# Optimization experiments

Measured on AMD Instinct MI355X. Metric: run time of the kernel, lower is better.

Reference implementation:

```python
import jax, jax.numpy as jnp
import numpy as np

EPS = 1e-6


def setup_inputs() -> dict:
    key = jax.random.key(0)
    kx, kw = jax.random.split(key)
    B, C, N = 8, 256, 2048
    x = jax.random.normal(kx, (B, C, N), dtype=jnp.float32)
    # nn.Linear(dim*2, 2, bias=False): weight shape [2, 2*C]
    W = jax.random.normal(kw, (2, 2 * C), dtype=jnp.float32) * (1.0 / np.sqrt(2 * C))
    return {"x": x, "W": W}


def reference(x, W):
    B, C, N = x.shape
    # cosine similarity matrix [B, N, N]
    sim = jnp.einsum('bcn,bcm->bnm', x, x)
    # torch: sqrt(sum(x^2 + 1e-6, dim=1)) -> eps added per-channel before sum
    norms = jnp.sqrt(jnp.sum(x * x + EPS, axis=1))            # [B, N]
    io_abs = sim / (norms[:, :, None] * norms[:, None, :])    # [B, N, N]
    # zero the diagonal (fill_diagonal_(0)) before argmax
    io_abs = io_abs * (1.0 - jnp.eye(N, dtype=io_abs.dtype))
    idx = jnp.argmax(io_abs, axis=2)                          # [B, N] nearest-neighbor per token
    # gather retrieved features: f_re[b, :, n] = x[b, :, idx[b, n]]
    f_re = jnp.take_along_axis(x, idx[:, None, :], axis=2)    # [B, C, N]
    # gated fusion
    fus = jnp.concatenate([x, f_re], axis=1).transpose(0, 2, 1)  # [B, N, 2C]
    w = jax.nn.softmax(fus @ W.T, axis=-1)                    # [B, N, 2]
    w = w.transpose(0, 2, 1)                                  # [B, 2, N]
    out = x * w[:, 0:1, :] + f_re * w[:, 1:2, :]
    return (out, f_re)
```

## Files before the change

kernel.cpp:

```cpp
#include <hip/hip_runtime.h>
#include <hip/hip_bf16.h>
#include <math.h>

constexpr int B_ = 8;
constexpr int C_ = 256;
constexpr int N_ = 2048;
constexpr int CN_ = C_ * N_;
constexpr int TOT_ = B_ * C_ * N_;
constexpr int NTILES = 16;
constexpr int NPAIRS = 136;

typedef __attribute__((ext_vector_type(8))) short bf16x8;
typedef __attribute__((ext_vector_type(4))) float f32x4;

__device__ __forceinline__ void g2l16(const void* g, void* l) {
    __builtin_amdgcn_global_load_lds(
        (const __attribute__((address_space(1))) void*)g,
        (__attribute__((address_space(3))) void*)l, 16, 0, 0);
}

__device__ __forceinline__ unsigned short bits(__hip_bfloat16 h) {
    union { __hip_bfloat16 b; unsigned short u; } cv;
    cv.b = h;
    return cv.u;
}

__device__ __forceinline__ float b2f(short s) {
    union { float f; unsigned u; } cv;
    cv.u = ((unsigned)(unsigned short)s) << 16;
    return cv.f;
}

__global__ __launch_bounds__(256) void convert_kernel(const float* __restrict__ x,
                                                      __hip_bfloat16* __restrict__ hiT,
                                                      __hip_bfloat16* __restrict__ loT,
                                                      float* __restrict__ normacc) {
    const int blk = blockIdx.x;
    const int batch = blk & 7;
    const int nt = (blk >> 3) & 31;
    const int ctile = blk >> 8;
    const int n0 = nt << 6, c0 = ctile << 6;
    const int t = threadIdx.x;
    const int i = t & 63, j = t >> 6;

    __shared__ float tb[64][65];
    __shared__ float red[4][64];

    float s = 0.f;
    const float* xp = x + (size_t)batch * CN_ + (size_t)c0 * N_ + n0 + i;
#pragma unroll 4
    for (int r = 0; r < 16; ++r) {
        const int cl = j + r * 4;
        const float v = xp[(size_t)cl * N_];
        tb[cl][i] = v;
        s += v * v;
    }
    red[j][i] = s;
    __syncthreads();

    const int cp = t & 31;
    const int c2 = cp << 1;
    const int nb = t >> 5;
#pragma unroll 4
    for (int r = 0; r < 8; ++r) {
        const int n = nb + r * 8;
        const float v0 = tb[c2][n], v1 = tb[c2 + 1][n];
        const size_t o = ((size_t)batch * N_ + n0 + n) * C_ + c0 + c2;
        const __hip_bfloat16 h0 = __float2bfloat16(v0);
        const __hip_bfloat16 h1 = __float2bfloat16(v1);
        const __hip_bfloat16 g0 = __float2bfloat16(v0 - __bfloat162float(h0));
        const __hip_bfloat16 g1 = __float2bfloat16(v1 - __bfloat162float(h1));
        ((unsigned*)hiT)[o >> 1] = ((unsigned)bits(h1) << 16) | bits(h0);
        ((unsigned*)loT)[o >> 1] = ((unsigned)bits(g1) << 16) | bits(g0);
    }
    if (j == 0) {
        const float tt = red[0][i] + red[1][i] + red[2][i] + red[3][i];
        atomicAdd(normacc + batch * N_ + n0 + i, tt);
    }
}

__global__ void rnorm_fin_kernel(const float* __restrict__ normacc,
                                 float* __restrict__ rnorm) {
    const int t = blockIdx.x * 256 + threadIdx.x;
    rnorm[t] = 1.0f / sqrtf(normacc[t] + 256.0f * 1e-6f);
}

__device__ __forceinline__ void stage_tile(const __hip_bfloat16* __restrict__ hiT,
                                           const __hip_bfloat16* __restrict__ loT,
                                           size_t base, int kb, short* dst, int tid) {
#pragma unroll
    for (int pp = 0; pp < 4; ++pp) {
        const int slot = tid + pp * 256;
        const int r = slot >> 3, sidx = slot & 7;
        const int sw = sidx ^ (r & 7);
        const size_t goff = base + (size_t)r * C_ + kb + (sw & 3) * 8;
        const __hip_bfloat16* src = (sw < 4) ? (hiT + goff) : (loT + goff);
        g2l16(src, dst + slot * 8);
    }
}

__global__ __launch_bounds__(256, 2) void gram_mfma_kernel(
        const __hip_bfloat16* __restrict__ hiT, const __hip_bfloat16* __restrict__ loT,
        const float* __restrict__ rnorm,
        float* __restrict__ pval, int* __restrict__ pidx, float* __restrict__ pval2) {
    const int blk = blockIdx.x;
    const int batch = blk & 7;
    int p = blk >> 3;
    int bn = 0;
    while (p >= NTILES - bn) { p -= NTILES - bn; ++bn; }
    const int bm = bn + p;
    const bool diag = (bn == bm);
    const int n0 = bn << 7, m0 = bm << 7;

    __shared__ short As[2][128 * 64];
    __shared__ short Bs[2][128 * 64];
    short* ov = &As[0][0];
    float (*rv1)[2] = (float(*)[2])(ov + 0);
    int (*ri1)[2] = (int(*)[2])(ov + 512);
    float (*rv2)[2] = (float(*)[2])(ov + 1024);
    float (*cv1)[2] = (float(*)[2])(ov + 1536);
    int (*ci1)[2] = (int(*)[2])(ov + 2048);
    float (*cv2)[2] = (float(*)[2])(ov + 2560);
    float* rnA = (float*)(ov + 3072);

    const int tid = threadIdx.x;
    const int l = tid & 63, w = tid >> 6;
    const int lm = l & 15, q = l >> 4;
    const int wn = (w >> 1) << 6, wm = (w & 1) << 6;

    f32x4 acc[4][4];
#pragma unroll
    for (int rt = 0; rt < 4; ++rt)
#pragma unroll
        for (int ct = 0; ct < 4; ++ct) acc[rt][ct] = (f32x4){0.f, 0.f, 0.f, 0.f};

    const size_t bbase = (size_t)batch * CN_;
    const size_t abase = bbase + (size_t)n0 * C_;
    const size_t bbase2 = bbase + (size_t)m0 * C_;

    stage_tile(hiT, loT, abase, 0, &As[0][0], tid);
    stage_tile(hiT, loT, bbase2, 0, &Bs[0][0], tid);
    __syncthreads();

    for (int kt = 0; kt < 8; ++kt) {
        const int cur = kt & 1;
        if (kt < 7) {
            const int kb = (kt + 1) << 5;
            stage_tile(hiT, loT, abase, kb, &As[cur ^ 1][0], tid);
            stage_tile(hiT, loT, bbase2, kb, &Bs[cur ^ 1][0], tid);
        }
        short* Ac = &As[cur][0];
        short* Bc = &Bs[cur][0];
        bf16x8 ah[4], al[4], bh[4], bl[4];
        const int x7 = lm & 7;
#pragma unroll
        for (int rt = 0; rt < 4; ++rt) {
            const int row = wn + rt * 16 + lm;
            ah[rt] = *(const bf16x8*)(Ac + row * 64 + ((q ^ x7) * 8));
            al[rt] = *(const bf16x8*)(Ac + row * 64 + (((4 | q) ^ x7) * 8));
        }
#pragma unroll
        for (int ct = 0; ct < 4; ++ct) {
            const int row = wm + ct * 16 + lm;
            bh[ct] = *(const bf16x8*)(Bc + row * 64 + ((q ^ x7) * 8));
            bl[ct] = *(const bf16x8*)(Bc + row * 64 + (((4 | q) ^ x7) * 8));
        }
#pragma unroll
        for (int rt = 0; rt < 4; ++rt)
#pragma unroll
            for (int ct = 0; ct < 4; ++ct) {
                acc[rt][ct] = __builtin_amdgcn_mfma_f32_16x16x32_bf16(
                    ah[rt], bh[ct], acc[rt][ct], 0, 0, 0);
                acc[rt][ct] = __builtin_amdgcn_mfma_f32_16x16x32_bf16(
                    ah[rt], bl[ct], acc[rt][ct], 0, 0, 0);
                acc[rt][ct] = __builtin_amdgcn_mfma_f32_16x16x32_bf16(
                    al[rt], bh[ct], acc[rt][ct], 0, 0, 0);
            }
        __syncthreads();
    }

    if (tid < 128) rnA[tid] = rnorm[batch * N_ + n0 + tid];

    float rnm[4];
#pragma unroll
    for (int ct = 0; ct < 4; ++ct) rnm[ct] = rnorm[batch * N_ + m0 + wm + ct * 16 + lm];

#pragma unroll
    for (int rt = 0; rt < 4; ++rt) {
#pragma unroll
        for (int r = 0; r < 4; ++r) {
            const int nrow = n0 + wn + rt * 16 + q * 4 + r;
            float v1 = -3.4e38f, v2 = -3.4e38f;
            int i1 = 0x7fffffff;
#pragma unroll
            for (int ct = 0; ct < 4; ++ct) {
                const int m = m0 + wm + ct * 16 + lm;
                const float v = acc[rt][ct][r] * rnm[ct];
                if (m == nrow) continue;
                if (v > v1) { v2 = v1; v1 = v; i1 = m; }
                else if (v > v2) v2 = v;
            }
#pragma unroll
            for (int d = 1; d < 16; d <<= 1) {
                const float ov1 = __shfl_xor(v1, d, 64);
                const int oi1 = __shfl_xor(i1, d, 64);
                const float ov2 = __shfl_xor(v2, d, 64);
                if (ov1 > v1 || (ov1 == v1 && oi1 < i1)) {
                    v2 = fmaxf(v1, ov2); v1 = ov1; i1 = oi1;
                } else {
                    v2 = fmaxf(v2, ov1);
                }
            }
            if (lm == 0) {
                const int rloc = wn + rt * 16 + q * 4 + r;
                rv1[rloc][w & 1] = v1;
                ri1[rloc][w & 1] = i1;
                rv2[rloc][w & 1] = v2;
            }
        }
    }
    __syncthreads();

    if (!diag) {
        float rnn[4][4];
#pragma unroll
        for (int rt = 0; rt < 4; ++rt)
#pragma unroll
            for (int r = 0; r < 4; ++r) rnn[rt][r] = rnA[wn + rt * 16 + q * 4 + r];
#pragma unroll
        for (int ct = 0; ct < 4; ++ct) {
            float v1 = -3.4e38f, v2 = -3.4e38f;
            int i1 = 0x7fffffff;
#pragma unroll
            for (int rt = 0; rt < 4; ++rt) {
#pragma unroll
                for (int r = 0; r < 4; ++r) {
                    const float v = acc[rt][ct][r] * rnn[rt][r];
                    const int nn = n0 + wn + rt * 16 + q * 4 + r;
                    if (v > v1) { v2 = v1; v1 = v; i1 = nn; }
                    else if (v > v2) v2 = v;
                }
            }
#pragma unroll
            for (int d = 16; d < 64; d <<= 1) {
                const float ov1 = __shfl_xor(v1, d, 64);
                const int oi1 = __shfl_xor(i1, d, 64);
                const float ov2 = __shfl_xor(v2, d, 64);
                if (ov1 > v1 || (ov1 == v1 && oi1 < i1)) {
                    v2 = fmaxf(v1, ov2); v1 = ov1; i1 = oi1;
                } else {
                    v2 = fmaxf(v2, ov1);
                }
            }
            if (q == 0) {
                const int mloc = wm + ct * 16 + lm;
                cv1[mloc][w >> 1] = v1;
                ci1[mloc][w >> 1] = i1;
                cv2[mloc][w >> 1] = v2;
            }
        }
    }
    __syncthreads();

    if (tid < 128) {
        {
            float v1 = rv1[tid][0]; int i1 = ri1[tid][0]; float v2 = rv2[tid][0];
            const float ov1 = rv1[tid][1]; const int oi1 = ri1[tid][1]; const float ov2 = rv2[tid][1];
            if (ov1 > v1 || (ov1 == v1 && oi1 < i1)) { v2 = fmaxf(v1, ov2); v1 = ov1; i1 = oi1; }
            else v2 = fmaxf(v2, ov1);
            const size_t gi = (size_t)(batch * NTILES + bm) * N_ + n0 + tid;
            pval[gi] = v1; pidx[gi] = i1; pval2[gi] = v2;
        }
        if (!diag) {
            float v1 = cv1[tid][0]; int i1 = ci1[tid][0]; float v2 = cv2[tid][0];
            const float ov1 = cv1[tid][1]; const int oi1 = ci1[tid][1]; const float ov2 = cv2[tid][1];
            if (ov1 > v1 || (ov1 == v1 && oi1 < i1)) { v2 = fmaxf(v1, ov2); v1 = ov1; i1 = oi1; }
            else v2 = fmaxf(v2, ov1);
            const size_t gi = (size_t)(batch * NTILES + bn) * N_ + m0 + tid;
            pval[gi] = v1; pidx[gi] = i1; pval2[gi] = v2;
        }
    }
}

__global__ void combine_kernel(const float* __restrict__ pval, const int* __restrict__ pidx,
                               const float* __restrict__ pval2, int* __restrict__ fidx,
                               int* __restrict__ rcnt, int* __restrict__ ridx) {
    const int t = blockIdx.x * 256 + threadIdx.x;
    const int batch = t >> 11, n = t & 2047;
    float v1 = -3.4e38f, v2 = -3.4e38f;
    int i1 = 0x7fffffff;
    for (int s = 0; s < NTILES; ++s) {
        const size_t gi = (size_t)(batch * NTILES + s) * N_ + n;
        const float ov1 = pval[gi]; const int oi1 = pidx[gi]; const float ov2 = pval2[gi];
        if (ov1 > v1 || (ov1 == v1 && oi1 < i1)) { v2 = fmaxf(v1, ov2); v1 = ov1; i1 = oi1; }
        else v2 = fmaxf(v2, ov1);
    }
    fidx[t] = i1;
    if (v1 - v2 < 1e-4f) {
        const int slot = atomicAdd(rcnt, 1);
        ridx[slot] = t;
    }
}

__global__ __launch_bounds__(256) void rescue_kernel(const float* __restrict__ x,
                                                     const float* __restrict__ rnorm,
                                                     const int* __restrict__ rcnt,
                                                     const int* __restrict__ ridx,
                                                     int* __restrict__ fidx) {
    const int cnt = *rcnt;
    const int tid = threadIdx.x;
    __shared__ float bv[256];
    __shared__ int bi[256];
    for (int rr = blockIdx.x; rr < cnt; rr += gridDim.x) {
        const int t = ridx[rr];
        const int batch = t >> 11, n = t & 2047;
        const float* xb = x + (size_t)batch * CN_;
        float s[8];
#pragma unroll
        for (int k = 0; k < 8; ++k) s[k] = 0.f;
        for (int c = 0; c < C_; ++c) {
            const float xc = xb[(size_t)c * N_ + n];
            const float* xr = xb + (size_t)c * N_;
#pragma unroll
            for (int k = 0; k < 8; ++k) s[k] += xc * xr[tid + (k << 8)];
        }
        float best = -3.4e38f;
        int besti = 0x7fffffff;
#pragma unroll
        for (int k = 0; k < 8; ++k) {
            const int m = tid + (k << 8);
            const float v = s[k] * rnorm[batch * N_ + m];
            if (m != n && v > best) { best = v; besti = m; }
        }
        bv[tid] = best; bi[tid] = besti;
        __syncthreads();
        for (int sft = 128; sft > 0; sft >>= 1) {
            if (tid < sft) {
                const float ov = bv[tid + sft]; const int oi = bi[tid + sft];
                if (ov > bv[tid] || (ov == bv[tid] && oi < bi[tid])) { bv[tid] = ov; bi[tid] = oi; }
            }
            __syncthreads();
        }
        if (tid == 0) fidx[t] = bi[0];
        __syncthreads();
    }
}

__global__ __launch_bounds__(256) void finish_kernel(const float* __restrict__ x,
                                                     const __hip_bfloat16* __restrict__ hiT,
                                                     const __hip_bfloat16* __restrict__ loT,
                                                     const float* __restrict__ W,
                                                     const int* __restrict__ fidx,
                                                     float* __restrict__ out) {
    const int batch = blockIdx.x & 7;
    const int nt = blockIdx.x >> 3;
    const int n0 = nt << 4;
    const int t = threadIdx.x;
    const int i = t & 15, cg = t >> 4;

    __shared__ float Wl[1024];
    __shared__ int il[16];
    __shared__ float l0r[16][17], l1r[16][17];
    __shared__ float w0s[16], w1s[16];

    for (int u = t; u < 1024; u += 256) Wl[u] = W[u];
    if (t < 16) il[t] = fidx[batch * N_ + n0 + t];
    __syncthreads();

    const float* xb = x + (size_t)batch * CN_ + n0 + i;
    const int myidx = il[i];
    const size_t row = ((size_t)batch * N_ + myidx) * C_ + cg * 16;

    float fvv[16];
    {
        const bf16x8* hp = (const bf16x8*)(hiT + row);
        const bf16x8* lp = (const bf16x8*)(loT + row);
#pragma unroll
        for (int v8 = 0; v8 < 2; ++v8) {
            const bf16x8 h = hp[v8];
            const bf16x8 g = lp[v8];
#pragma unroll
            for (int e = 0; e < 8; ++e) fvv[v8 * 8 + e] = b2f(h[e]) + b2f(g[e]);
        }
    }

    float l0 = 0.f, l1 = 0.f;
#pragma unroll
    for (int cc = 0; cc < 16; ++cc) {
        const int c = cg * 16 + cc;
        const float xv = xb[(size_t)c * N_];
        l0 += xv * Wl[c] + fvv[cc] * Wl[256 + c];
        l1 += xv * Wl[512 + c] + fvv[cc] * Wl[768 + c];
    }
    l0r[cg][i] = l0;
    l1r[cg][i] = l1;
    __syncthreads();
    if (t < 16) {
        float L0 = 0.f, L1 = 0.f;
#pragma unroll
        for (int g = 0; g < 16; ++g) { L0 += l0r[g][t]; L1 += l1r[g][t]; }
        const float mx = fmaxf(L0, L1);
        const float e0 = expf(L0 - mx);
        const float e1 = expf(L1 - mx);
        const float inv = 1.0f / (e0 + e1);
        w0s[t] = e0 * inv;
        w1s[t] = e1 * inv;
    }
    __syncthreads();
    const float w0 = w0s[i], w1 = w1s[i];

#pragma unroll
    for (int cc = 0; cc < 16; ++cc) {
        const int c = cg * 16 + cc;
        const size_t off = (size_t)batch * CN_ + (size_t)c * N_ + n0 + i;
        const float xv = xb[(size_t)c * N_];
        out[off] = xv * w0 + fvv[cc] * w1;
        out[TOT_ + off] = fvv[cc];
    }
}

extern "C" void kernel_launch(void* const* d_in, const int* in_sizes, int n_in,
                              void* d_out, int out_size, void* d_ws, size_t ws_size,
                              hipStream_t stream) {
    const float* x = (const float*)d_in[0];
    const float* W = (const float*)d_in[1];
    float* out = (float*)d_out;

    const size_t BF_BYTES = (size_t)TOT_ * 2;
    const size_t NORM_BYTES = (size_t)B_ * N_ * 4;
    const size_t P_BYTES = (size_t)B_ * NTILES * N_ * 4;

    uint8_t* p = (uint8_t*)d_ws;
    __hip_bfloat16* hiT = (__hip_bfloat16*)p; p += BF_BYTES;
    __hip_bfloat16* loT = (__hip_bfloat16*)p; p += BF_BYTES;
    float* rnorm = (float*)p; p += NORM_BYTES;
    float* normacc = (float*)p; p += NORM_BYTES;
    float* pval = (float*)p; p += P_BYTES;
    int* pidx = (int*)p; p += P_BYTES;
    float* pval2 = (float*)p; p += P_BYTES;
    int* fidx = (int*)p; p += NORM_BYTES;
    int* rcnt = (int*)p; p += 256;
    int* ridx = (int*)p; p += NORM_BYTES;

    hipMemsetAsync(rcnt, 0, 4, stream);
    hipMemsetAsync(normacc, 0, NORM_BYTES, stream);
    convert_kernel<<<1024, 256, 0, stream>>>(x, hiT, loT, normacc);
    rnorm_fin_kernel<<<64, 256, 0, stream>>>(normacc, rnorm);
    gram_mfma_kernel<<<B_ * NPAIRS, 256, 0, stream>>>(hiT, loT, rnorm, pval, pidx, pval2);
    combine_kernel<<<64, 256, 0, stream>>>(pval, pidx, pval2, fidx, rcnt, ridx);
    rescue_kernel<<<64, 256, 0, stream>>>(x, rnorm, rcnt, ridx, fidx);
    finish_kernel<<<1024, 256, 0, stream>>>(x, hiT, loT, W, fidx, out);
}
```

Measured before the change: 200.8 us.

## Split rescue argmax across column chunks with packed atomicMax keys; precompute gram addresses

The rescue pass now splits each ambiguous row into 8 column chunks of 256 and spreads them over 256 blocks instead of 64. Each block reduces a packed 64-bit key (order-preserving float bits plus inverted index), merges it into a per-row result with atomicMax, and a new finalize kernel decodes the winning index. The gram kernel also precomputes its global and LDS staging addresses and fully unrolls the k loop over explicit double buffers to reduce address arithmetic. This adds an extra kernel launch and atomics in exchange for more parallelism in the rescue stage.

```diff
diff --git a/kernel.cpp b/kernel.cpp
--- a/kernel.cpp
+++ b/kernel.cpp
@@ -29,6 +29,12 @@
     union { float f; unsigned u; } cv;
     cv.u = ((unsigned)(unsigned short)s) << 16;
     return cv.f;
+}
+
+__device__ __forceinline__ unsigned long long packkey(float v, int m) {
+    const unsigned b = __float_as_uint(v);
+    const unsigned u = (b & 0x80000000u) ? ~b : (b | 0x80000000u);
+    return ((unsigned long long)u << 32) | (unsigned)(2047 - m);
 }
 
 __global__ __launch_bounds__(256) void convert_kernel(const float* __restrict__ x,
@@ -85,20 +91,6 @@
     rnorm[t] = 1.0f / sqrtf(normacc[t] + 256.0f * 1e-6f);
 }
 
-__device__ __forceinline__ void stage_tile(const __hip_bfloat16* __restrict__ hiT,
-                                           const __hip_bfloat16* __restrict__ loT,
-                                           size_t base, int kb, short* dst, int tid) {
-#pragma unroll
-    for (int pp = 0; pp < 4; ++pp) {
-        const int slot = tid + pp * 256;
-        const int r = slot >> 3, sidx = slot & 7;
-        const int sw = sidx ^ (r & 7);
-        const size_t goff = base + (size_t)r * C_ + kb + (sw & 3) * 8;
-        const __hip_bfloat16* src = (sw < 4) ? (hiT + goff) : (loT + goff);
-        g2l16(src, dst + slot * 8);
-    }
-}
-
 __global__ __launch_bounds__(256, 2) void gram_mfma_kernel(
         const __hip_bfloat16* __restrict__ hiT, const __hip_bfloat16* __restrict__ loT,
         const float* __restrict__ rnorm,
@@ -112,9 +104,11 @@
     const bool diag = (bn == bm);
     const int n0 = bn << 7, m0 = bm << 7;
 
-    __shared__ short As[2][128 * 64];
-    __shared__ short Bs[2][128 * 64];
-    short* ov = &As[0][0];
+    __shared__ short As0[128 * 64];
+    __shared__ short As1[128 * 64];
+    __shared__ short Bs0[128 * 64];
+    __shared__ short Bs1[128 * 64];
+    short* ov = &As0[0];
     float (*rv1)[2] = (float(*)[2])(ov + 0);
     int (*ri1)[2] = (int(*)[2])(ov + 512);
     float (*rv2)[2] = (float(*)[2])(ov + 1024);
@@ -126,44 +120,70 @@
     const int tid = threadIdx.x;
     const int l = tid & 63, w = tid >> 6;
     const int lm = l & 15, q = l >> 4;
+    const int x7 = lm & 7;
     const int wn = (w >> 1) << 6, wm = (w & 1) << 6;
 
+    const size_t bbase = (size_t)batch * CN_;
+    const short* gA[4];
+    const short* gB[4];
+    int ldsoff[4];
+#pragma unroll
+    for (int pp = 0; pp < 4; ++pp) {
+        const int slot = tid + pp * 256;
+        const int r = slot >> 3, sidx = slot & 7;
+        const int sw = sidx ^ (r & 7);
+        const short* base = (const short*)((sw < 4) ? hiT : loT);
+        gA[pp] = base + bbase + (size_t)(n0 + r) * C_ + (sw & 3) * 8;
+        gB[pp] = base + bbase + (size_t)(m0 + r) * C_ + (sw & 3) * 8;
+        ldsoff[pp] = slot * 8;
+    }
+    int aoff[8], boff[8];
+#pragma unroll
+    for (int rt = 0; rt < 4; ++rt) {
+        const int ra = wn + rt * 16 + lm;
+        const int rb = wm + rt * 16 + lm;
+        aoff[rt * 2] = ra * 64 + ((q ^ x7) * 8);
+        aoff[rt * 2 + 1] = ra * 64 + (((4 | q) ^ x7) * 8);
+        boff[rt * 2] = rb * 64 + ((q ^ x7) * 8);
+        boff[rt * 2 + 1] = rb * 64 + (((4 | q) ^ x7) * 8);
+    }
+
     f32x4 acc[4][4];
 #pragma unroll
     for (int rt = 0; rt < 4; ++rt)
 #pragma unroll
         for (int ct = 0; ct < 4; ++ct) acc[rt][ct] = (f32x4){0.f, 0.f, 0.f, 0.f};
 
-    const size_t bbase = (size_t)batch * CN_;
-    const size_t abase = bbase + (size_t)n0 * C_;
-    const size_t bbase2 = bbase + (size_t)m0 * C_;
-
-    stage_tile(hiT, loT, abase, 0, &As[0][0], tid);
-    stage_tile(hiT, loT, bbase2, 0, &Bs[0][0], tid);
-    __syncthreads();
-
+#pragma unroll
+    for (int pp = 0; pp < 4; ++pp) {
+        g2l16(gA[pp], As0 + ldsoff[pp]);
+        g2l16(gB[pp], Bs0 + ldsoff[pp]);
+    }
+    __syncthreads();
+
+#pragma unroll
     for (int kt = 0; kt < 8; ++kt) {
-        const int cur = kt & 1;
+        short* Ac = (kt & 1) ? As1 : As0;
+        short* Bc = (kt & 1) ? Bs1 : Bs0;
         if (kt < 7) {
-            const int kb = (kt + 1) << 5;
-            stage_tile(hiT, loT, abase, kb, &As[cur ^ 1][0], tid);
-            stage_tile(hiT, loT, bbase2, kb, &Bs[cur ^ 1][0], tid);
-        }
-        short* Ac = &As[cur][0];
-        short* Bc = &Bs[cur][0];
+            short* An = (kt & 1) ? As0 : As1;
+            short* Bn = (kt & 1) ? Bs0 : Bs1;
+#pragma unroll
+            for (int pp = 0; pp < 4; ++pp) {
+                g2l16(gA[pp] + (kt + 1) * 32, An + ldsoff[pp]);
+                g2l16(gB[pp] + (kt + 1) * 32, Bn + ldsoff[pp]);
+            }
+        }
         bf16x8 ah[4], al[4], bh[4], bl[4];
-        const int x7 = lm & 7;
 #pragma unroll
         for (int rt = 0; rt < 4; ++rt) {
-            const int row = wn + rt * 16 + lm;
-            ah[rt] = *(const bf16x8*)(Ac + row * 64 + ((q ^ x7) * 8));
-            al[rt] = *(const bf16x8*)(Ac + row * 64 + (((4 | q) ^ x7) * 8));
+            ah[rt] = *(const bf16x8*)(Ac + aoff[rt * 2]);
+            al[rt] = *(const bf16x8*)(Ac + aoff[rt * 2 + 1]);
         }
 #pragma unroll
         for (int ct = 0; ct < 4; ++ct) {
-            const int row = wm + ct * 16 + lm;
-            bh[ct] = *(const bf16x8*)(Bc + row * 64 + ((q ^ x7) * 8));
-            bl[ct] = *(const bf16x8*)(Bc + row * 64 + (((4 | q) ^ x7) * 8));
+            bh[ct] = *(const bf16x8*)(Bc + boff[ct * 2]);
+            bl[ct] = *(const bf16x8*)(Bc + boff[ct * 2 + 1]);
         }
 #pragma unroll
         for (int rt = 0; rt < 4; ++rt)
@@ -284,7 +304,8 @@
 
 __global__ void combine_kernel(const float* __restrict__ pval, const int* __restrict__ pidx,
                                const float* __restrict__ pval2, int* __restrict__ fidx,
-                               int* __restrict__ rcnt, int* __restrict__ ridx) {
+                               int* __restrict__ rcnt, int* __restrict__ ridx,
+                               unsigned long long* __restrict__ pbest) {
     const int t = blockIdx.x * 256 + threadIdx.x;
     const int batch = t >> 11, n = t & 2047;
     float v1 = -3.4e38f, v2 = -3.4e38f;
@@ -299,6 +320,7 @@
     if (v1 - v2 < 1e-4f) {
         const int slot = atomicAdd(rcnt, 1);
         ridx[slot] = t;
+        pbest[slot] = 0ull;
     }
 }
 
@@ -306,43 +328,51 @@
                                                      const float* __restrict__ rnorm,
                                                      const int* __restrict__ rcnt,
                                                      const int* __restrict__ ridx,
-                                                     int* __restrict__ fidx) {
+                                                     unsigned long long* __restrict__ pbest) {
     const int cnt = *rcnt;
+    const int nwork = cnt << 3;
     const int tid = threadIdx.x;
-    __shared__ float bv[256];
-    __shared__ int bi[256];
-    for (int rr = blockIdx.x; rr < cnt; rr += gridDim.x) {
+    __shared__ unsigned long long bk[256];
+    for (int wi = blockIdx.x; wi < nwork; wi += gridDim.x) {
+        const int rr = wi >> 3, ch = wi & 7;
         const int t = ridx[rr];
         const int batch = t >> 11, n = t & 2047;
+        const int m = (ch << 8) + tid;
         const float* xb = x + (size_t)batch * CN_;
-        float s[8];
-#pragma unroll
-        for (int k = 0; k < 8; ++k) s[k] = 0.f;
-        for (int c = 0; c < C_; ++c) {
-            const float xc = xb[(size_t)c * N_ + n];
-            const float* xr = xb + (size_t)c * N_;
-#pragma unroll
-            for (int k = 0; k < 8; ++k) s[k] += xc * xr[tid + (k << 8)];
-        }
-        float best = -3.4e38f;
-        int besti = 0x7fffffff;
-#pragma unroll
-        for (int k = 0; k < 8; ++k) {
-            const int m = tid + (k << 8);
-            const float v = s[k] * rnorm[batch * N_ + m];
-            if (m != n && v > best) { best = v; besti = m; }
-        }
-        bv[tid] = best; bi[tid] = besti;
+        float s0 = 0.f, s1 = 0.f, s2 = 0.f, s3 = 0.f;
+        const float* xn = xb + n;
+        const float* xm = xb + m;
+#pragma unroll 4
+        for (int c = 0; c < C_; c += 4) {
+            s0 += xn[(size_t)(c + 0) * N_] * xm[(size_t)(c + 0) * N_];
+            s1 += xn[(size_t)(c + 1) * N_] * xm[(size_t)(c + 1) * N_];
+            s2 += xn[(size_t)(c + 2) * N_] * xm[(size_t)(c + 2) * N_];
+            s3 += xn[(size_t)(c + 3) * N_] * xm[(size_t)(c + 3) * N_];
+        }
+        const float v = ((s0 + s1) + (s2 + s3)) * rnorm[batch * N_ + m];
+        bk[tid] = (m == n) ? 0ull : packkey(v, m);
         __syncthreads();
         for (int sft = 128; sft > 0; sft >>= 1) {
             if (tid < sft) {
-                const float ov = bv[tid + sft]; const int oi = bi[tid + sft];
-                if (ov > bv[tid] || (ov == bv[tid] && oi < bi[tid])) { bv[tid] = ov; bi[tid] = oi; }
+                const unsigned long long o = bk[tid + sft];
+                if (o > bk[tid]) bk[tid] = o;
             }
             __syncthreads();
         }
-        if (tid == 0) fidx[t] = bi[0];
+        if (tid == 0) atomicMax(&pbest[rr], bk[0]);
         __syncthreads();
+    }
+}
+
+__global__ void rescue_fin_kernel(const unsigned long long* __restrict__ pbest,
+                                  const int* __restrict__ rcnt,
+                                  const int* __restrict__ ridx,
+                                  int* __restrict__ fidx) {
+    const int rr = blockIdx.x * 256 + threadIdx.x;
+    if (rr < *rcnt) {
+        const unsigned long long k = pbest[rr];
+        const int m = 2047 - (int)(unsigned)(k & 0xffffffffull);
+        fidx[ridx[rr]] = m;
     }
 }
 
@@ -441,13 +471,15 @@
     int* fidx = (int*)p; p += NORM_BYTES;
     int* rcnt = (int*)p; p += 256;
     int* ridx = (int*)p; p += NORM_BYTES;
+    unsigned long long* pbest = (unsigned long long*)p; p += (size_t)B_ * N_ * 8;
 
     hipMemsetAsync(rcnt, 0, 4, stream);
     hipMemsetAsync(normacc, 0, NORM_BYTES, stream);
     convert_kernel<<<1024, 256, 0, stream>>>(x, hiT, loT, normacc);
     rnorm_fin_kernel<<<64, 256, 0, stream>>>(normacc, rnorm);
     gram_mfma_kernel<<<B_ * NPAIRS, 256, 0, stream>>>(hiT, loT, rnorm, pval, pidx, pval2);
-    combine_kernel<<<64, 256, 0, stream>>>(pval, pidx, pval2, fidx, rcnt, ridx);
-    rescue_kernel<<<64, 256, 0, stream>>>(x, rnorm, rcnt, ridx, fidx);
+    combine_kernel<<<64, 256, 0, stream>>>(pval, pidx, pval2, fidx, rcnt, ridx, pbest);
+    rescue_kernel<<<256, 256, 0, stream>>>(x, rnorm, rcnt, ridx, pbest);
+    rescue_fin_kernel<<<64, 256, 0, stream>>>(pbest, rcnt, ridx, fidx);
     finish_kernel<<<1024, 256, 0, stream>>>(x, hiT, loT, W, fidx, out);
 }
```

Result: faster. 180.3 us (-10.2%).
